# Kernel optimization log

Hardware: AMD Instinct MI355X
Metric: run time of the kernel (lower is better)

Reference implementation:

```python
import jax, jax.numpy as jnp
import numpy as np

DIM = 128


def setup_inputs() -> dict:
    key = jax.random.key(0)
    k1, k2, k3, k4 = jax.random.split(key, 4)
    x = jax.random.normal(k1, (8, 32768, DIM), dtype=jnp.float32)
    # nn.Linear(dim, dim*3, bias=False): weight applied as x @ W.T; store as [dim, 3*dim]
    W_qkv = jax.random.normal(k2, (DIM, 3 * DIM), dtype=jnp.float32) * (DIM ** -0.5)
    W_out = jax.random.normal(k3, (DIM, DIM), dtype=jnp.float32) * (DIM ** -0.5)
    b_out = jax.random.normal(k4, (DIM,), dtype=jnp.float32) * 0.01
    return {"x": x, "W_qkv": W_qkv, "W_out": W_out, "b_out": b_out}


def reference(x, W_qkv, W_out, b_out):
    dim = x.shape[-1]
    scale = dim ** -0.5
    qkv = x @ W_qkv  # [b, n, 3d]
    q, k, v = jnp.split(qkv, 3, axis=-1)
    q = jax.nn.softmax(q, axis=-1) * scale
    k = jax.nn.softmax(k, axis=-1)
    v = jax.nn.softmax(v, axis=-1)
    context = jnp.einsum('bnd,bne->bde', q, k)  # [b, d, d]
    out = jnp.einsum('bde,bne->bnd', context, v)  # [b, n, d]
    return out @ W_out + b_out
```

## Files before the change

### kernel.cpp

```cpp
#include <hip/hip_runtime.h>

#define SEQ 32768
#define QSCALE 0.08838834764831845f
#define NCH 16

typedef __attribute__((ext_vector_type(8))) short short8;
typedef __attribute__((ext_vector_type(8))) __bf16 bf16x8;
typedef __attribute__((ext_vector_type(16))) float f32x16;
typedef __attribute__((ext_vector_type(4))) float f32x4;
typedef __attribute__((ext_vector_type(4))) int int4v;
typedef __attribute__((ext_vector_type(2))) int int2v;

#define SWZ(r, c) ((((r) << 7) + (c)) ^ (((r) & 15) << 3))
#define PSWZ(ch, n) ((((ch) << 6) + (n)) ^ (((ch) & 7) << 3))

__device__ __forceinline__ int cvtpk(float lo, float hi) {
  int r;
  asm("v_cvt_pk_bf16_f32 %0, %1, %2" : "=v"(r) : "v"(lo), "v"(hi));
  return r;
}

__device__ __forceinline__ short bf16b(float f) {
  unsigned u = __builtin_bit_cast(unsigned, f);
  u += 0x7fffu + ((u >> 16) & 1u);
  return (short)(u >> 16);
}

__device__ __forceinline__ f32x16 mfma_ii(int4v a, int4v b, f32x16 c) {
  return __builtin_amdgcn_mfma_f32_32x32x16_bf16(
      __builtin_bit_cast(bf16x8, a), __builtin_bit_cast(bf16x8, b), c, 0, 0, 0);
}

__device__ __forceinline__ int4v build_frag(float e0, float e1, float e2, float e3,
                                            float e4, float e5, float e6, float e7,
                                            int hi) {
  int t0 = cvtpk(e0, e1), t1 = cvtpk(e2, e3);
  int t2 = cvtpk(e4, e5), t3 = cvtpk(e6, e7);
  const int u0 = __shfl_xor(t2, 32), u1 = __shfl_xor(t3, 32);
  const int u2 = __shfl_xor(t0, 32), u3 = __shfl_xor(t1, 32);
  int4v f;
  f[0] = hi ? u0 : t0;
  f[1] = hi ? u1 : t1;
  f[2] = hi ? t2 : u2;
  f[3] = hi ? t3 : u3;
  return f;
}

__global__ void la_prep(const float* __restrict__ Wqkv, int4v* __restrict__ Wf) {
  const int fid = blockIdx.x * 256 + threadIdx.x;
  if (fid >= 6144) return;
  const int side = fid >> 11;
  const int rem = fid & 2047;
  const int tile = rem >> 9;
  const int ks = (rem >> 6) & 7;
  const int lane = rem & 63;
  const int k0 = ks * 16 + ((lane >> 5) << 3);
  const int col = side * 128 + tile * 32 + (lane & 31);
  int4v f;
  #pragma unroll
  for (int a = 0; a < 4; ++a)
    f[a] = cvtpk(Wqkv[(k0 + 2 * a) * 384 + col], Wqkv[(k0 + 2 * a + 1) * 384 + col]);
  Wf[fid] = f;
}

__global__ __launch_bounds__(1024, 4)
void la_pass1(const float* __restrict__ x, const int4v* __restrict__ Wf,
              float* __restrict__ partials) {
  __shared__ __align__(16) short xs[2][64 * 128];
  __shared__ __align__(16) short ptile[2][2][128 * 64];
  __shared__ __align__(16) float sumbuf[2][2][2][32][4];

  const int tid = threadIdx.x;
  const int lane = tid & 63;
  const int wv = tid >> 6;
  const int l31 = lane & 31;
  const int hi = lane >> 5;
  const int koff = hi << 3;
  const int h = wv >> 3;
  const int c = (wv >> 1) & 3;
  const int rh = wv & 1;
  const int td = wv >> 2;
  const int te = wv & 3;
  const int b = blockIdx.x >> 5;
  const int strip = blockIdx.x & 31;
  const long base = (long)b * SEQ + (long)strip * (NCH * 64);

  int4v wf[8];
  #pragma unroll
  for (int ks = 0; ks < 8; ++ks)
    wf[ks] = Wf[((((h << 2) + c) << 3) + ks) * 64 + lane];

  const int lr = tid >> 4;
  const int cf = (tid & 15) << 3;
  {
    const float* xp = x + (base + lr) * 128 + cf;
    f32x4 u0 = *(const f32x4*)xp;
    f32x4 u1 = *(const f32x4*)(xp + 4);
    int4v p;
    p[0] = cvtpk(u0[0], u0[1]); p[1] = cvtpk(u0[2], u0[3]);
    p[2] = cvtpk(u1[0], u1[1]); p[3] = cvtpk(u1[2], u1[3]);
    *(int4v*)&xs[0][SWZ(lr, cf)] = p;
  }
  __syncthreads();

  f32x16 ctx = {0.f};
  const int r0 = rh << 5;
  for (int i = 0; i < NCH; ++i) {
    const int cur = i & 1;
    const int inx = (i + 1 < NCH) ? i + 1 : i;
    const float* xp = x + (base + inx * 64 + lr) * 128 + cf;
    f32x4 u0 = *(const f32x4*)xp;
    f32x4 u1 = *(const f32x4*)(xp + 4);

    f32x16 acc = {0.f};
    #pragma unroll
    for (int ks = 0; ks < 8; ++ks) {
      const int4v xf = *(const int4v*)&xs[cur][SWZ(r0 + l31, (ks << 4) + koff)];
      acc = mfma_ii(wf[ks], xf, acc);
    }
    {
      float sa = 0.f, sb = 0.f;
      #pragma unroll
      for (int r = 0; r < 16; r += 2) {
        acc[r] = __expf(acc[r]);         sa += acc[r];
        acc[r + 1] = __expf(acc[r + 1]); sb += acc[r + 1];
      }
      float s = sa + sb;
      s += __shfl_xor(s, 32);
      if (!hi) sumbuf[cur][h][rh][l31][c] = s;
    }

    {
      int4v p;
      p[0] = cvtpk(u0[0], u0[1]); p[1] = cvtpk(u0[2], u0[3]);
      p[2] = cvtpk(u1[0], u1[1]); p[3] = cvtpk(u1[2], u1[3]);
      *(int4v*)&xs[cur ^ 1][SWZ(lr, cf)] = p;
    }
    __syncthreads();

    if (i > 0) {
      const int pb = cur ^ 1;
      #pragma unroll
      for (int ks = 0; ks < 4; ++ks) {
        const int4v aq = *(const int4v*)&ptile[pb][0][PSWZ((td << 5) + l31, (ks << 4) + koff)];
        const int4v bk = *(const int4v*)&ptile[pb][1][PSWZ((te << 5) + l31, (ks << 4) + koff)];
        ctx = mfma_ii(aq, bk, ctx);
      }
    }

    {
      short* pt = &ptile[cur][h][0];
      const int n = (rh << 5) + l31;
      if (h == 0) {
        const f32x4 sq = *(const f32x4*)&sumbuf[cur][0][rh][l31][0];
        const f32x4 sk = *(const f32x4*)&sumbuf[cur][1][rh][l31][0];
        const float invn = QSCALE * __builtin_amdgcn_rcpf(
            (sq[0] + sq[1] + sq[2] + sq[3]) * (sk[0] + sk[1] + sk[2] + sk[3]));
        #pragma unroll
        for (int r = 0; r < 16; ++r) {
          const int ch = (c << 5) + (r & 3) + ((r >> 2) << 3) + (hi << 2);
          pt[PSWZ(ch, n)] = bf16b(acc[r] * invn);
        }
      } else {
        #pragma unroll
        for (int r = 0; r < 16; ++r) {
          const int ch = (c << 5) + (r & 3) + ((r >> 2) << 3) + (hi << 2);
          pt[PSWZ(ch, n)] = bf16b(acc[r]);
        }
      }
    }
  }
  __syncthreads();
  {
    const int pb = (NCH - 1) & 1;
    #pragma unroll
    for (int ks = 0; ks < 4; ++ks) {
      const int4v aq = *(const int4v*)&ptile[pb][0][PSWZ((td << 5) + l31, (ks << 4) + koff)];
      const int4v bk = *(const int4v*)&ptile[pb][1][PSWZ((te << 5) + l31, (ks << 4) + koff)];
      ctx = mfma_ii(aq, bk, ctx);
    }
  }

  float* pout = partials + (long)blockIdx.x * 16384;
  #pragma unroll
  for (int r = 0; r < 16; ++r) {
    const int drow = (td << 5) + (r & 3) + ((r >> 2) << 3) + (hi << 2);
    pout[(drow << 7) + (te << 5) + l31] = ctx[r];
  }
}

__global__ void la_reduce(const float* __restrict__ partials, float* __restrict__ ctx,
                          int strips) {
  const int b = blockIdx.x >> 4;
  const int sl = blockIdx.x & 15;
  const int idx = (sl << 10) + ((int)threadIdx.x << 2);
  f32x4 acc = {0.f};
  for (int st = 0; st < strips; ++st)
    acc += *(const f32x4*)(partials + ((long)(b * strips + st) << 14) + idx);
  *(f32x4*)(ctx + ((long)b << 14) + idx) = acc;
}

__global__ void la_mkern(const float* __restrict__ ctx, const float* __restrict__ Wout,
                         int4v* __restrict__ Mtf) {
  __shared__ __align__(16) float cl[128 * 132];
  __shared__ float wo[128 * 32];
  const int tid = threadIdx.x;
  const int b = blockIdx.x >> 2;
  const int d0 = (blockIdx.x & 3) << 5;
  const float* cp = ctx + ((long)b << 14);
  for (int i = tid << 2; i < 16384; i += 1024) {
    f32x4 v = *(const f32x4*)(cp + i);
    *(f32x4*)&cl[(i >> 7) * 132 + (i & 127)] = v;
  }
  for (int i = tid; i < 128 * 32; i += 256)
    wo[i] = Wout[((i >> 5) << 7) + d0 + (i & 31)];
  __syncthreads();
  const int dq = tid >> 3;
  const int e0 = (tid & 7) << 4;
  float acc[16];
  #pragma unroll
  for (int i = 0; i < 16; ++i) acc[i] = 0.0f;
  for (int d = 0; d < 128; ++d) {
    const float w = wo[(d << 5) + dq];
    const float* cr = &cl[d * 132 + e0];
    #pragma unroll
    for (int i = 0; i < 16; ++i) acc[i] += cr[i] * w;
  }
  const int dp = d0 + dq;
  const int j = dp & 3, l = dp >> 2, ks = e0 >> 4;
  int4v lo, hi2;
  lo[0] = cvtpk(acc[0], acc[1]);   lo[1] = cvtpk(acc[2], acc[3]);
  lo[2] = cvtpk(acc[4], acc[5]);   lo[3] = cvtpk(acc[6], acc[7]);
  hi2[0] = cvtpk(acc[8], acc[9]);  hi2[1] = cvtpk(acc[10], acc[11]);
  hi2[2] = cvtpk(acc[12], acc[13]); hi2[3] = cvtpk(acc[14], acc[15]);
  int4v* dst = Mtf + ((((long)b << 2) + j) * 8 + ks) * 64;
  dst[l] = lo;
  dst[32 + l] = hi2;
}

__global__ __launch_bounds__(256, 3)
void la_pass2(const float* __restrict__ x, const int4v* __restrict__ Wf,
              const int4v* __restrict__ Mtf, const float* __restrict__ bout,
              float* __restrict__ out) {
  __shared__ __align__(16) short xs[4][32 * 128];

  const int tid = threadIdx.x;
  const int lane = tid & 63;
  const int wv = tid >> 6;
  const int l31 = lane & 31;
  const int hi = lane >> 5;
  const int koff = hi << 3;
  const int b = blockIdx.x >> 8;
  const int chunk = blockIdx.x & 255;
  const long row0 = (long)b * SEQ + (long)chunk * 128 + (wv << 5);

  {
    const float* xb = x + row0 * 128;
    f32x4 uA[8];
    #pragma unroll
    for (int t = 0; t < 8; ++t)
      uA[t] = *(const f32x4*)(xb + t * 256 + lane * 4);
    f32x4 uB[8];
    #pragma unroll
    for (int t = 0; t < 8; ++t)
      uB[t] = *(const f32x4*)(xb + (t + 8) * 256 + lane * 4);
    #pragma unroll
    for (int t = 0; t < 8; ++t) {
      const int flat = t * 256 + lane * 4;
      int2v w;
      w[0] = cvtpk(uA[t][0], uA[t][1]);
      w[1] = cvtpk(uA[t][2], uA[t][3]);
      *(int2v*)&xs[wv][SWZ(flat >> 7, flat & 127)] = w;
    }
    #pragma unroll
    for (int t = 0; t < 8; ++t) {
      const int flat = (t + 8) * 256 + lane * 4;
      int2v w;
      w[0] = cvtpk(uB[t][0], uB[t][1]);
      w[1] = cvtpk(uB[t][2], uB[t][3]);
      *(int2v*)&xs[wv][SWZ(flat >> 7, flat & 127)] = w;
    }
  }
  const f32x4 bias = *(const f32x4*)(bout + (l31 << 2));
  asm volatile("s_waitcnt lgkmcnt(0)" ::: "memory");
  __builtin_amdgcn_sched_barrier(0);

  int4v xfr[8];
  #pragma unroll
  for (int ks = 0; ks < 8; ++ks)
    xfr[ks] = *(const int4v*)&xs[wv][SWZ(l31, (ks << 4) + koff)];

  const int4v* WvT = Wf + 2 * 2048;
  f32x16 a0 = {0.f}, a1 = {0.f}, a2 = {0.f}, a3 = {0.f};
  #pragma unroll
  for (int ks = 0; ks < 8; ++ks) {
    a0 = mfma_ii(WvT[(0 * 8 + ks) * 64 + lane], xfr[ks], a0);
    a1 = mfma_ii(WvT[(1 * 8 + ks) * 64 + lane], xfr[ks], a1);
    a2 = mfma_ii(WvT[(2 * 8 + ks) * 64 + lane], xfr[ks], a2);
    a3 = mfma_ii(WvT[(3 * 8 + ks) * 64 + lane], xfr[ks], a3);
  }

  float s = 0.f;
  #pragma unroll
  for (int r = 0; r < 16; ++r) {
    a0[r] = __expf(a0[r]); s += a0[r];
    a1[r] = __expf(a1[r]); s += a1[r];
    a2[r] = __expf(a2[r]); s += a2[r];
    a3[r] = __expf(a3[r]); s += a3[r];
  }
  s += __shfl_xor(s, 32);
  const float inv = __builtin_amdgcn_rcpf(s);
  #pragma unroll
  for (int r = 0; r < 16; ++r) {
    a0[r] *= inv; a1[r] *= inv; a2[r] *= inv; a3[r] *= inv;
  }

  const int4v* MtB = Mtf + ((long)b << 11);
  f32x16 o0 = {0.f}, o1 = {0.f}, o2 = {0.f}, o3 = {0.f};
#define OUT_T(T, AT)                                                          \
  {                                                                           \
    const int4v f0 = build_frag(AT[0], AT[1], AT[2], AT[3],                   \
                                AT[4], AT[5], AT[6], AT[7], hi);              \
    o0 = mfma_ii(f0, MtB[(0 * 8 + 2 * T) * 64 + lane], o0);                   \
    o1 = mfma_ii(f0, MtB[(1 * 8 + 2 * T) * 64 + lane], o1);                   \
    o2 = mfma_ii(f0, MtB[(2 * 8 + 2 * T) * 64 + lane], o2);                   \
    o3 = mfma_ii(f0, MtB[(3 * 8 + 2 * T) * 64 + lane], o3);                   \
    const int4v f1 = build_frag(AT[8], AT[9], AT[10], AT[11],                 \
                                AT[12], AT[13], AT[14], AT[15], hi);          \
    o0 = mfma_ii(f1, MtB[(0 * 8 + 2 * T + 1) * 64 + lane], o0);               \
    o1 = mfma_ii(f1, MtB[(1 * 8 + 2 * T + 1) * 64 + lane], o1);               \
    o2 = mfma_ii(f1, MtB[(2 * 8 + 2 * T + 1) * 64 + lane], o2);               \
    o3 = mfma_ii(f1, MtB[(3 * 8 + 2 * T + 1) * 64 + lane], o3);               \
  }
  OUT_T(0, a0)
  OUT_T(1, a1)
  OUT_T(2, a2)
  OUT_T(3, a3)
#undef OUT_T

  float* obase = out + row0 * 128 + (l31 << 2);
  #pragma unroll
  for (int r = 0; r < 16; ++r) {
    const int n = (r & 3) + ((r >> 2) << 3) + (hi << 2);
    f32x4 v;
    v[0] = o0[r] + bias[0];
    v[1] = o1[r] + bias[1];
    v[2] = o2[r] + bias[2];
    v[3] = o3[r] + bias[3];
    *(f32x4*)(obase + (long)n * 128) = v;
  }
}

extern "C" void kernel_launch(void* const* d_in, const int* in_sizes, int n_in,
                              void* d_out, int out_size, void* d_ws, size_t ws_size,
                              hipStream_t stream) {
  const float* x = (const float*)d_in[0];
  const float* Wqkv = (const float*)d_in[1];
  const float* Wout = (const float*)d_in[2];
  const float* bout = (const float*)d_in[3];
  float* out = (float*)d_out;

  const int strips = 32;

  float* partials = (float*)d_ws;
  float* ctx = partials + (size_t)8 * strips * 16384;
  int4v* Mtf = (int4v*)(ctx + 8 * 16384);
  int4v* Wf = Mtf + 16384;

  la_prep<<<dim3(24), dim3(256), 0, stream>>>(Wqkv, Wf);
  la_pass1<<<dim3(8 * strips), dim3(1024), 0, stream>>>(x, Wf, partials);
  la_reduce<<<dim3(128), dim3(256), 0, stream>>>(partials, ctx, strips);
  la_mkern<<<dim3(32), dim3(256), 0, stream>>>(ctx, Wout, Mtf);
  la_pass2<<<dim3(2048), dim3(256), 0, stream>>>(x, Wf, Mtf, bout, out);
}
```

Before: 149.9 us.

## Split pass1 into more, smaller blocks with 32-row chunks

The context-accumulation kernel now uses 512-thread blocks that each process 32-row chunks. Each wave accumulates two 32x32 context tiles, and the ptile buffer is single-buffered with padded rows instead of an XOR swizzle. The strip count rises to 64 when the workspace is large enough, doubling the grid so more blocks spread across CUs. In exchange, it drops the overlap of the context MFMAs with the next chunk's projection, adds a barrier per chunk, and doubles the partials written and reduced.

```diff
diff --git a/kernel.cpp b/kernel.cpp
--- a/kernel.cpp
+++ b/kernel.cpp
@@ -2,7 +2,6 @@
 
 #define SEQ 32768
 #define QSCALE 0.08838834764831845f
-#define NCH 16
 
 typedef __attribute__((ext_vector_type(8))) short short8;
 typedef __attribute__((ext_vector_type(8))) __bf16 bf16x8;
@@ -12,7 +11,6 @@
 typedef __attribute__((ext_vector_type(2))) int int2v;
 
 #define SWZ(r, c) ((((r) << 7) + (c)) ^ (((r) & 15) << 3))
-#define PSWZ(ch, n) ((((ch) << 6) + (n)) ^ (((ch) & 7) << 3))
 
 __device__ __forceinline__ int cvtpk(float lo, float hi) {
   int r;
@@ -63,12 +61,12 @@
   Wf[fid] = f;
 }
 
-__global__ __launch_bounds__(1024, 4)
+__global__ __launch_bounds__(512, 4)
 void la_pass1(const float* __restrict__ x, const int4v* __restrict__ Wf,
-              float* __restrict__ partials) {
-  __shared__ __align__(16) short xs[2][64 * 128];
-  __shared__ __align__(16) short ptile[2][2][128 * 64];
-  __shared__ __align__(16) float sumbuf[2][2][2][32][4];
+              float* __restrict__ partials, int strips, int nch) {
+  __shared__ __align__(16) short xs[2][32 * 128];
+  __shared__ __align__(16) short ptile[2][128 * 40];
+  __shared__ __align__(16) float sumbuf[2][32][4];
 
   const int tid = threadIdx.x;
   const int lane = tid & 63;
@@ -76,14 +74,13 @@
   const int l31 = lane & 31;
   const int hi = lane >> 5;
   const int koff = hi << 3;
-  const int h = wv >> 3;
-  const int c = (wv >> 1) & 3;
-  const int rh = wv & 1;
-  const int td = wv >> 2;
-  const int te = wv & 3;
-  const int b = blockIdx.x >> 5;
-  const int strip = blockIdx.x & 31;
-  const long base = (long)b * SEQ + (long)strip * (NCH * 64);
+  const int h = wv >> 2;
+  const int c = wv & 3;
+  const int td = wv >> 1;
+  const int teb = (wv & 1) << 1;
+  const int b = blockIdx.x / strips;
+  const int strip = blockIdx.x - b * strips;
+  const long base = (long)b * SEQ + (long)strip * (nch * 32);
 
   int4v wf[8];
   #pragma unroll
@@ -103,19 +100,18 @@
   }
   __syncthreads();
 
-  f32x16 ctx = {0.f};
-  const int r0 = rh << 5;
-  for (int i = 0; i < NCH; ++i) {
+  f32x16 ctx0 = {0.f}, ctx1 = {0.f};
+  for (int i = 0; i < nch; ++i) {
     const int cur = i & 1;
-    const int inx = (i + 1 < NCH) ? i + 1 : i;
-    const float* xp = x + (base + inx * 64 + lr) * 128 + cf;
+    const int inx = (i + 1 < nch) ? i + 1 : i;
+    const float* xp = x + (base + inx * 32 + lr) * 128 + cf;
     f32x4 u0 = *(const f32x4*)xp;
     f32x4 u1 = *(const f32x4*)(xp + 4);
 
     f32x16 acc = {0.f};
     #pragma unroll
     for (int ks = 0; ks < 8; ++ks) {
-      const int4v xf = *(const int4v*)&xs[cur][SWZ(r0 + l31, (ks << 4) + koff)];
+      const int4v xf = *(const int4v*)&xs[cur][SWZ(l31, (ks << 4) + koff)];
       acc = mfma_ii(wf[ks], xf, acc);
     }
     {
@@ -127,7 +123,7 @@
       }
       float s = sa + sb;
       s += __shfl_xor(s, 32);
-      if (!hi) sumbuf[cur][h][rh][l31][c] = s;
+      if (!hi) sumbuf[h][l31][c] = s;
     }
 
     {
@@ -138,46 +134,34 @@
     }
     __syncthreads();
 
-    if (i > 0) {
-      const int pb = cur ^ 1;
-      #pragma unroll
-      for (int ks = 0; ks < 4; ++ks) {
-        const int4v aq = *(const int4v*)&ptile[pb][0][PSWZ((td << 5) + l31, (ks << 4) + koff)];
-        const int4v bk = *(const int4v*)&ptile[pb][1][PSWZ((te << 5) + l31, (ks << 4) + koff)];
-        ctx = mfma_ii(aq, bk, ctx);
-      }
-    }
-
     {
-      short* pt = &ptile[cur][h][0];
-      const int n = (rh << 5) + l31;
+      short* pt = &ptile[h][0];
       if (h == 0) {
-        const f32x4 sq = *(const f32x4*)&sumbuf[cur][0][rh][l31][0];
-        const f32x4 sk = *(const f32x4*)&sumbuf[cur][1][rh][l31][0];
+        const f32x4 sq = *(const f32x4*)&sumbuf[0][l31][0];
+        const f32x4 sk = *(const f32x4*)&sumbuf[1][l31][0];
         const float invn = QSCALE * __builtin_amdgcn_rcpf(
             (sq[0] + sq[1] + sq[2] + sq[3]) * (sk[0] + sk[1] + sk[2] + sk[3]));
         #pragma unroll
         for (int r = 0; r < 16; ++r) {
           const int ch = (c << 5) + (r & 3) + ((r >> 2) << 3) + (hi << 2);
-          pt[PSWZ(ch, n)] = bf16b(acc[r] * invn);
+          pt[ch * 40 + l31] = bf16b(acc[r] * invn);
         }
       } else {
         #pragma unroll
         for (int r = 0; r < 16; ++r) {
           const int ch = (c << 5) + (r & 3) + ((r >> 2) << 3) + (hi << 2);
-          pt[PSWZ(ch, n)] = bf16b(acc[r]);
+          pt[ch * 40 + l31] = bf16b(acc[r]);
         }
       }
     }
-  }
-  __syncthreads();
-  {
-    const int pb = (NCH - 1) & 1;
-    #pragma unroll
-    for (int ks = 0; ks < 4; ++ks) {
-      const int4v aq = *(const int4v*)&ptile[pb][0][PSWZ((td << 5) + l31, (ks << 4) + koff)];
-      const int4v bk = *(const int4v*)&ptile[pb][1][PSWZ((te << 5) + l31, (ks << 4) + koff)];
-      ctx = mfma_ii(aq, bk, ctx);
+    __syncthreads();
+
+    #pragma unroll
+    for (int ks = 0; ks < 2; ++ks) {
+      const int kk = (ks << 4) + koff;
+      const int4v aq = *(const int4v*)&ptile[0][((td << 5) + l31) * 40 + kk];
+      ctx0 = mfma_ii(aq, *(const int4v*)&ptile[1][((teb << 5) + l31) * 40 + kk], ctx0);
+      ctx1 = mfma_ii(aq, *(const int4v*)&ptile[1][(((teb + 1) << 5) + l31) * 40 + kk], ctx1);
     }
   }
 
@@ -185,7 +169,8 @@
   #pragma unroll
   for (int r = 0; r < 16; ++r) {
     const int drow = (td << 5) + (r & 3) + ((r >> 2) << 3) + (hi << 2);
-    pout[(drow << 7) + (te << 5) + l31] = ctx[r];
+    pout[(drow << 7) + (teb << 5) + l31] = ctx0[r];
+    pout[(drow << 7) + ((teb + 1) << 5) + l31] = ctx1[r];
   }
 }
 
@@ -360,7 +345,9 @@
   const float* bout = (const float*)d_in[3];
   float* out = (float*)d_out;
 
-  const int strips = 32;
+  const size_t fixed = (size_t)8 * 16384 * 4 + (size_t)16384 * 16 + (size_t)6144 * 16;
+  const int strips = (ws_size >= (size_t)8 * 64 * 16384 * 4 + fixed) ? 64 : 32;
+  const int nch = SEQ / (strips * 32);
 
   float* partials = (float*)d_ws;
   float* ctx = partials + (size_t)8 * strips * 16384;
@@ -368,7 +355,7 @@
   int4v* Wf = Mtf + 16384;
 
   la_prep<<<dim3(24), dim3(256), 0, stream>>>(Wqkv, Wf);
-  la_pass1<<<dim3(8 * strips), dim3(1024), 0, stream>>>(x, Wf, partials);
+  la_pass1<<<dim3(8 * strips), dim3(512), 0, stream>>>(x, Wf, partials, strips, nch);
   la_reduce<<<dim3(128), dim3(256), 0, stream>>>(partials, ctx, strips);
   la_mkern<<<dim3(32), dim3(256), 0, stream>>>(ctx, Wout, Mtf);
   la_pass2<<<dim3(2048), dim3(256), 0, stream>>>(x, Wf, Mtf, bout, out);
```

Measured after the change: 150.7 us. Within noise of the previous version (+0.5%).

## Split pass2 output GEMM into two halves to cut registers and raise occupancy

Applied to the files above, without the earlier changes.

Reorders the Mtf fragment layout so output columns are grouped into two 64-column halves with interleaved pairs. Pass2 then computes and stores each half with only two accumulators live at once instead of four, using 8-byte stores. The launch bound rises from 3 to 4 waves per SIMD to use the freed registers. The cost is narrower, less coalesced output stores and a layout change that must match between the producer and consumer kernels.

```diff
diff --git a/kernel.cpp b/kernel.cpp
--- a/kernel.cpp
+++ b/kernel.cpp
@@ -8,6 +8,7 @@
 typedef __attribute__((ext_vector_type(8))) __bf16 bf16x8;
 typedef __attribute__((ext_vector_type(16))) float f32x16;
 typedef __attribute__((ext_vector_type(4))) float f32x4;
+typedef __attribute__((ext_vector_type(2))) float f32x2;
 typedef __attribute__((ext_vector_type(4))) int int4v;
 typedef __attribute__((ext_vector_type(2))) int int2v;
 
@@ -227,18 +228,18 @@
     for (int i = 0; i < 16; ++i) acc[i] += cr[i] * w;
   }
   const int dp = d0 + dq;
-  const int j = dp & 3, l = dp >> 2, ks = e0 >> 4;
+  const int half = dp >> 6, jj = dp & 1, ll = (dp >> 1) & 31, ks = e0 >> 4;
   int4v lo, hi2;
   lo[0] = cvtpk(acc[0], acc[1]);   lo[1] = cvtpk(acc[2], acc[3]);
   lo[2] = cvtpk(acc[4], acc[5]);   lo[3] = cvtpk(acc[6], acc[7]);
   hi2[0] = cvtpk(acc[8], acc[9]);  hi2[1] = cvtpk(acc[10], acc[11]);
   hi2[2] = cvtpk(acc[12], acc[13]); hi2[3] = cvtpk(acc[14], acc[15]);
-  int4v* dst = Mtf + ((((long)b << 2) + j) * 8 + ks) * 64;
-  dst[l] = lo;
-  dst[32 + l] = hi2;
-}
-
-__global__ __launch_bounds__(256, 3)
+  int4v* dst = Mtf + (long)b * 2048 + half * 1024 + jj * 512 + ks * 64;
+  dst[ll] = lo;
+  dst[32 + ll] = hi2;
+}
+
+__global__ __launch_bounds__(256, 4)
 void la_pass2(const float* __restrict__ x, const int4v* __restrict__ Wf,
               const int4v* __restrict__ Mtf, const float* __restrict__ bout,
               float* __restrict__ out) {
@@ -281,7 +282,8 @@
       *(int2v*)&xs[wv][SWZ(flat >> 7, flat & 127)] = w;
     }
   }
-  const f32x4 bias = *(const f32x4*)(bout + (l31 << 2));
+  const f32x2 bA = *(const f32x2*)(bout + (l31 << 1));
+  const f32x2 bB = *(const f32x2*)(bout + 64 + (l31 << 1));
   asm volatile("s_waitcnt lgkmcnt(0)" ::: "memory");
   __builtin_amdgcn_sched_barrier(0);
 
@@ -316,39 +318,49 @@
   }
 
   const int4v* MtB = Mtf + ((long)b << 11);
-  f32x16 o0 = {0.f}, o1 = {0.f}, o2 = {0.f}, o3 = {0.f};
-#define OUT_T(T, AT)                                                          \
-  {                                                                           \
-    const int4v f0 = build_frag(AT[0], AT[1], AT[2], AT[3],                   \
-                                AT[4], AT[5], AT[6], AT[7], hi);              \
-    o0 = mfma_ii(f0, MtB[(0 * 8 + 2 * T) * 64 + lane], o0);                   \
-    o1 = mfma_ii(f0, MtB[(1 * 8 + 2 * T) * 64 + lane], o1);                   \
-    o2 = mfma_ii(f0, MtB[(2 * 8 + 2 * T) * 64 + lane], o2);                   \
-    o3 = mfma_ii(f0, MtB[(3 * 8 + 2 * T) * 64 + lane], o3);                   \
-    const int4v f1 = build_frag(AT[8], AT[9], AT[10], AT[11],                 \
-                                AT[12], AT[13], AT[14], AT[15], hi);          \
-    o0 = mfma_ii(f1, MtB[(0 * 8 + 2 * T + 1) * 64 + lane], o0);               \
-    o1 = mfma_ii(f1, MtB[(1 * 8 + 2 * T + 1) * 64 + lane], o1);               \
-    o2 = mfma_ii(f1, MtB[(2 * 8 + 2 * T + 1) * 64 + lane], o2);               \
-    o3 = mfma_ii(f1, MtB[(3 * 8 + 2 * T + 1) * 64 + lane], o3);               \
-  }
-  OUT_T(0, a0)
-  OUT_T(1, a1)
-  OUT_T(2, a2)
-  OUT_T(3, a3)
-#undef OUT_T
-
-  float* obase = out + row0 * 128 + (l31 << 2);
-  #pragma unroll
-  for (int r = 0; r < 16; ++r) {
-    const int n = (r & 3) + ((r >> 2) << 3) + (hi << 2);
-    f32x4 v;
-    v[0] = o0[r] + bias[0];
-    v[1] = o1[r] + bias[1];
-    v[2] = o2[r] + bias[2];
-    v[3] = o3[r] + bias[3];
-    *(f32x4*)(obase + (long)n * 128) = v;
-  }
+  float* obase = out + row0 * 128 + (l31 << 1);
+#define OUT_T2(BASE, T, AT, O0, O1)                                            \
+  {                                                                            \
+    const int4v f0 = build_frag(AT[0], AT[1], AT[2], AT[3],                    \
+                                AT[4], AT[5], AT[6], AT[7], hi);               \
+    O0 = mfma_ii(f0, MtB[(BASE) + (2 * T) * 64 + lane], O0);                   \
+    O1 = mfma_ii(f0, MtB[(BASE) + 512 + (2 * T) * 64 + lane], O1);             \
+    const int4v f1 = build_frag(AT[8], AT[9], AT[10], AT[11],                  \
+                                AT[12], AT[13], AT[14], AT[15], hi);           \
+    O0 = mfma_ii(f1, MtB[(BASE) + (2 * T + 1) * 64 + lane], O0);               \
+    O1 = mfma_ii(f1, MtB[(BASE) + 512 + (2 * T + 1) * 64 + lane], O1);         \
+  }
+  {
+    f32x16 o0 = {0.f}, o1 = {0.f};
+    OUT_T2(0, 0, a0, o0, o1)
+    OUT_T2(0, 1, a1, o0, o1)
+    OUT_T2(0, 2, a2, o0, o1)
+    OUT_T2(0, 3, a3, o0, o1)
+    #pragma unroll
+    for (int r = 0; r < 16; ++r) {
+      const int n = (r & 3) + ((r >> 2) << 3) + (hi << 2);
+      f32x2 v;
+      v[0] = o0[r] + bA[0];
+      v[1] = o1[r] + bA[1];
+      *(f32x2*)(obase + (long)n * 128) = v;
+    }
+  }
+  {
+    f32x16 o2 = {0.f}, o3 = {0.f};
+    OUT_T2(1024, 0, a0, o2, o3)
+    OUT_T2(1024, 1, a1, o2, o3)
+    OUT_T2(1024, 2, a2, o2, o3)
+    OUT_T2(1024, 3, a3, o2, o3)
+    #pragma unroll
+    for (int r = 0; r < 16; ++r) {
+      const int n = (r & 3) + ((r >> 2) << 3) + (hi << 2);
+      f32x2 v;
+      v[0] = o2[r] + bB[0];
+      v[1] = o3[r] + bB[1];
+      *(f32x2*)(obase + 64 + (long)n * 128) = v;
+    }
+  }
+#undef OUT_T2
 }
 
 extern "C" void kernel_launch(void* const* d_in, const int* in_sizes, int n_in,
```

New measurement: 144.0 us. 4.0% less time.
